# Kernel optimization log

Measured on AMD Instinct MI355X. Metric: run time of the kernel, lower is better.

Reference implementation:

```python
import jax, jax.numpy as jnp
import numpy as np

S, B, D = 2048, 2, 1024
H = 16
DH = D // H
FF = 4096
EPS = 1e-5


def _layernorm(x, g, b):
    mu = jnp.mean(x, axis=-1, keepdims=True)
    var = jnp.var(x, axis=-1, keepdims=True)
    return (x - mu) * jax.lax.rsqrt(var + EPS) * g + b


def setup_inputs() -> dict:
    key = jax.random.key(0)
    ks = jax.random.split(key, 8)
    scale = 1.0 / np.sqrt(D)
    return {
        "x": jax.random.normal(ks[0], (S, B, D), dtype=jnp.float32),
        "wq": jax.random.normal(ks[1], (D, D), dtype=jnp.float32) * scale,
        "wk": jax.random.normal(ks[2], (D, D), dtype=jnp.float32) * scale,
        "wv": jax.random.normal(ks[3], (D, D), dtype=jnp.float32) * scale,
        "wo": jax.random.normal(ks[4], (D, D), dtype=jnp.float32) * scale,
        "ln1_g": jnp.ones((D,), jnp.float32),
        "ln1_b": jnp.zeros((D,), jnp.float32),
        "ln2_g": jnp.ones((D,), jnp.float32),
        "ln2_b": jnp.zeros((D,), jnp.float32),
        "w1": jax.random.normal(ks[5], (D, FF), dtype=jnp.float32) * scale,
        "b1": jnp.zeros((FF,), jnp.float32),
        "w2": jax.random.normal(ks[6], (FF, D), dtype=jnp.float32) * (1.0 / np.sqrt(FF)),
        "b2": jnp.zeros((D,), jnp.float32),
    }


def reference(x, wq, wk, wv, wo, ln1_g, ln1_b, ln2_g, ln2_b, w1, b1, w2, b2):
    # --- sublayer 0: pre-LN multi-head self-attention with residual ---
    # original loops per timestep with mask=False, i.e. full (non-causal)
    # attention over the whole sequence; vectorized here.
    y = _layernorm(x, ln1_g, ln1_b)                      # [S,B,D]
    q = (y @ wq).reshape(S, B, H, DH)
    k = (y @ wk).reshape(S, B, H, DH)
    v = (y @ wv).reshape(S, B, H, DH)
    scores = jnp.einsum("sbhd,tbhd->bhst", q, k) / np.sqrt(DH)  # [B,H,S,S]
    attn = jax.nn.softmax(scores, axis=-1)
    ctx = jnp.einsum("bhst,tbhd->sbhd", attn, v).reshape(S, B, D)
    x = x + ctx @ wo

    # --- sublayer 1: pre-LN position-wise FFN with residual ---
    z = _layernorm(x, ln2_g, ln2_b)
    h = jax.nn.relu(z @ w1 + b1)
    return x + h @ w2 + b2
```

## Files before the change

### kernel.cpp

```cpp
#include <hip/hip_runtime.h>
#include <hip/hip_bf16.h>
#include <stdint.h>


#define S_LEN 2048
#define BATCH 2
#define DMODEL 1024
#define NHEAD 16
#define DHEAD 64
#define FFDIM 4096
#define MROWS (S_LEN * BATCH)

typedef unsigned short u16;
typedef __attribute__((ext_vector_type(8))) __bf16 bf16x8;
typedef __attribute__((ext_vector_type(4))) float f32x4;
typedef __attribute__((ext_vector_type(4))) u16 u16x4;

__device__ inline u16 f2bf(float f) {
  union { float f; unsigned u; } v; v.f = f;
  unsigned r = v.u + 0x7fffu + ((v.u >> 16) & 1u);
  return (u16)(r >> 16);
}

__device__ inline f32x4 mfma16(bf16x8 a, bf16x8 b, f32x4 c) {
  return __builtin_amdgcn_mfma_f32_16x16x32_bf16(a, b, c, 0, 0, 0);
}

__device__ inline void gload_lds16(const u16* g, u16* l) {
  __builtin_amdgcn_global_load_lds(
      (const __attribute__((address_space(1))) unsigned int*)g,
      (__attribute__((address_space(3))) unsigned int*)l, 16, 0, 0);
}

__device__ inline uint32_t cvt_pk_bf16(float lo, float hi) {
  uint32_t r;
  asm("v_cvt_pk_bf16_f32 %0, %1, %2" : "=v"(r) : "v"(lo), "v"(hi));
  return r;
}

__global__ __launch_bounds__(256) void ln_kernel(const float* __restrict__ x,
                                                 const float* __restrict__ gam,
                                                 const float* __restrict__ bet,
                                                 u16* __restrict__ out) {
  int row = blockIdx.x;
  int tid = threadIdx.x;
  const float4* xr = (const float4*)(x + (size_t)row * DMODEL);
  float4 v = xr[tid];
  float s = v.x + v.y + v.z + v.w;
  float ss = v.x * v.x + v.y * v.y + v.z * v.z + v.w * v.w;
#pragma unroll
  for (int m = 1; m < 64; m <<= 1) {
    s += __shfl_xor(s, m);
    ss += __shfl_xor(ss, m);
  }
  __shared__ float red[8];
  int w = tid >> 6, lane = tid & 63;
  if (lane == 0) { red[w] = s; red[4 + w] = ss; }
  __syncthreads();
  s = red[0] + red[1] + red[2] + red[3];
  ss = red[4] + red[5] + red[6] + red[7];
  float mu = s * (1.f / DMODEL);
  float var = ss * (1.f / DMODEL) - mu * mu;
  float rstd = rsqrtf(var + 1e-5f);
  float4 gv = ((const float4*)gam)[tid];
  float4 bv = ((const float4*)bet)[tid];
  u16x4 o;
  o.x = f2bf((v.x - mu) * rstd * gv.x + bv.x);
  o.y = f2bf((v.y - mu) * rstd * gv.y + bv.y);
  o.z = f2bf((v.z - mu) * rstd * gv.z + bv.z);
  o.w = f2bf((v.w - mu) * rstd * gv.w + bv.w);
  *(u16x4*)(out + (size_t)row * DMODEL + tid * 4) = o;
}

__global__ __launch_bounds__(256) void transpose_all(const float* __restrict__ wq,
                                                     const float* __restrict__ wk,
                                                     const float* __restrict__ wv,
                                                     const float* __restrict__ wo,
                                                     const float* __restrict__ w1,
                                                     const float* __restrict__ w2,
                                                     u16* __restrict__ wqkvt, u16* __restrict__ wot,
                                                     u16* __restrict__ w1t, u16* __restrict__ w2t) {
  int idx = blockIdx.x;
  const float* in;
  u16* out;
  int R, C;
  if (idx < 3072) {
    int which = idx >> 10;
    in = (which == 0) ? wq : (which == 1) ? wk : wv;
    out = wqkvt + (size_t)which * 1024 * 1024;
    R = 1024; C = 1024;
    idx &= 1023;
  } else if (idx < 4096) {
    in = wo; out = wot; R = 1024; C = 1024; idx -= 3072;
  } else if (idx < 8192) {
    in = w1; out = w1t; R = 1024; C = 4096; idx -= 4096;
  } else {
    in = w2; out = w2t; R = 4096; C = 1024; idx -= 8192;
  }
  int ntx = C >> 5;
  int tc = idx % ntx, tr = idx / ntx;
  int c0 = tc * 32, r0 = tr * 32;
  __shared__ u16 tile[32][33];
  int tx = threadIdx.x & 31, grp = threadIdx.x >> 5;
#pragma unroll
  for (int i = 0; i < 4; i++) {
    int r = grp * 4 + i;
    tile[r][tx] = f2bf(in[(size_t)(r0 + r) * C + c0 + tx]);
  }
  __syncthreads();
#pragma unroll
  for (int i = 0; i < 4; i++) {
    int rr = grp * 4 + i;
    out[(size_t)(c0 + rr) * R + r0 + tx] = tile[tx][rr];
  }
}

__global__ __launch_bounds__(256) void transpose_v(const u16* __restrict__ qkv,
                                                   u16* __restrict__ vt) {
  __shared__ u16 tile[32][33];
  int bh = blockIdx.z;
  int b = bh >> 4;
  int s0 = blockIdx.x * 32, d0 = blockIdx.y * 32;
  int h = bh & 15;
  int tx = threadIdx.x & 31, grp = threadIdx.x >> 5;
#pragma unroll
  for (int i = 0; i < 4; i++) {
    int sl = grp * 4 + i;
    tile[sl][tx] = qkv[(size_t)((s0 + sl) * BATCH + b) * 3072 + 2048 + h * DHEAD + d0 + tx];
  }
  __syncthreads();
#pragma unroll
  for (int i = 0; i < 4; i++) {
    int dl = grp * 4 + i;
    vt[((size_t)bh * DHEAD + d0 + dl) * S_LEN + s0 + tx] = tile[tx][dl];
  }
}

template <int MODE, int BN>
__global__ __launch_bounds__(256) void gemm_bt(const u16* __restrict__ A,
                                               const u16* __restrict__ Bt, void* __restrict__ Cout,
                                               const float* __restrict__ bias,
                                               const float* __restrict__ res, int M, int N, int K) {
  __shared__ __align__(16) u16 As[2][128 * 64];
  __shared__ __align__(16) u16 Bs[2][BN * 64];
  constexpr int NLOADS = 4 + BN / 32;

  int nwg = gridDim.x * gridDim.y;
  int f = blockIdx.y * gridDim.x + blockIdx.x;
  int nf = ((nwg & 7) == 0) ? ((f & 7) * (nwg >> 3) + (f >> 3)) : f;
  int bx = nf % gridDim.x, by = nf / gridDim.x;

  int bm0 = by * 128, bn0 = bx * BN;
  int tid = threadIdx.x, w = tid >> 6, lane = tid & 63;
  int g = lane >> 4, l15 = lane & 15;
  int lr = lane >> 3, ch = lane & 7;
  int srcch = (ch ^ lr) * 8;
  int wm = (w >> 1) * 64, wn = (w & 1) * (BN / 2);
  const int NJ = BN / 32;

  f32x4 acc[4][NJ];
#pragma unroll
  for (int i = 0; i < 4; i++)
#pragma unroll
    for (int j = 0; j < NJ; j++) {
      f32x4 z = {0.f, 0.f, 0.f, 0.f};
      acc[i][j] = z;
    }

  auto stage = [&](int k0, int buf) {
#pragma unroll
    for (int rd = 0; rd < 4; rd++) {
      int rb = (rd * 4 + w) * 8;
      gload_lds16(A + (size_t)(bm0 + rb + lr) * K + k0 + srcch, &As[buf][rb * 64]);
    }
#pragma unroll
    for (int rd = 0; rd < BN / 32; rd++) {
      int rb = (rd * 4 + w) * 8;
      gload_lds16(Bt + (size_t)(bn0 + rb + lr) * K + k0 + srcch, &Bs[buf][rb * 64]);
    }
  };

  int nkt = K >> 6;
  stage(0, 0);
  asm volatile("s_waitcnt vmcnt(0)" ::: "memory");
  __builtin_amdgcn_s_barrier();

  for (int kt = 0; kt < nkt; ++kt) {
    int cur = kt & 1;
    if (kt + 1 < nkt) {
      stage((kt + 1) << 6, cur ^ 1);
      asm volatile("s_waitcnt vmcnt(%0)" ::"n"(NLOADS) : "memory");
    } else {
      asm volatile("s_waitcnt vmcnt(0)" ::: "memory");
    }
    __builtin_amdgcn_s_barrier();
#pragma unroll
    for (int kk = 0; kk < 2; kk++) {
      bf16x8 af[4], bfr[NJ];
#pragma unroll
      for (int i = 0; i < 4; i++) {
        int row = wm + i * 16 + l15;
        af[i] = *(const bf16x8*)&As[cur][row * 64 + (((kk * 4 + g) ^ (row & 7)) * 8)];
      }
#pragma unroll
      for (int j = 0; j < NJ; j++) {
        int row = wn + j * 16 + l15;
        bfr[j] = *(const bf16x8*)&Bs[cur][row * 64 + (((kk * 4 + g) ^ (row & 7)) * 8)];
      }
#pragma unroll
      for (int i = 0; i < 4; i++)
#pragma unroll
        for (int j = 0; j < NJ; j++) acc[i][j] = mfma16(af[i], bfr[j], acc[i][j]);
    }
    __builtin_amdgcn_s_barrier();
  }

#pragma unroll
  for (int i = 0; i < 4; i++)
#pragma unroll
    for (int j = 0; j < NJ; j++) {
      int col = bn0 + wn + j * 16 + l15;
      float bval = (MODE == 2 || MODE == 3) ? bias[col] : 0.f;
#pragma unroll
      for (int r = 0; r < 4; r++) {
        int row = bm0 + wm + i * 16 + g * 4 + r;
        size_t idx = (size_t)row * N + col;
        float vacc = acc[i][j][r] + bval;
        if (MODE == 0)
          ((u16*)Cout)[idx] = f2bf(vacc);
        else if (MODE == 1)
          ((float*)Cout)[idx] = vacc + res[idx];
        else if (MODE == 2)
          ((u16*)Cout)[idx] = f2bf(fmaxf(vacc, 0.f));
        else
          ((float*)Cout)[idx] = vacc + res[idx];
      }
    }
}

__global__ __launch_bounds__(256) void attn_kernel(const u16* __restrict__ qkv,
                                                   const u16* __restrict__ vt,
                                                   u16* __restrict__ ctx) {
  int nwg = gridDim.x * gridDim.y;
  int f = blockIdx.y * gridDim.x + blockIdx.x;
  int nf = (f & 7) * (nwg >> 3) + (f >> 3);
  int qblk = nf % gridDim.x, bh = nf / gridDim.x;
  int b = bh >> 4, h = bh & 15;
  int tid = threadIdx.x, w = tid >> 6, lane = tid & 63;
  int g = lane >> 4, l15 = lane & 15;
  int lr = lane >> 3, ch = lane & 7;
  int q0 = qblk * 64 + w * 16;
  const float SCALE = 0.125f * 1.44269504f;

  __shared__ __align__(16) u16 ks[2][64 * 64];
  __shared__ __align__(16) u16 vs[2][64 * 64];

  bf16x8 qf0, qf1;
  {
    const u16* qp = qkv + ((size_t)(q0 + l15) * BATCH + b) * 3072 + h * DHEAD;
    qf0 = *(const bf16x8*)(qp + g * 8);
    qf1 = *(const bf16x8*)(qp + 32 + g * 8);
  }
  bf16x8 onef;
  {
    union { u16 u[8]; bf16x8 v; } ou;
#pragma unroll
    for (int i = 0; i < 8; i++) ou.u[i] = 0x3F80;
    onef = ou.v;
  }

  f32x4 accT[4];
#pragma unroll
  for (int n = 0; n < 4; n++) {
    f32x4 z = {0.f, 0.f, 0.f, 0.f};
    accT[n] = z;
  }
  f32x4 lacc = {0.f, 0.f, 0.f, 0.f};
  float negms = 0.f;

  auto stage = [&](int t0, int buf) {
#pragma unroll
    for (int rd = 0; rd < 2; rd++) {
      int rb = w * 16 + rd * 8;
      int row = rb + lr;
      const u16* ksrc =
          qkv + ((size_t)(t0 + row) * BATCH + b) * 3072 + 1024 + h * DHEAD + (ch ^ lr) * 8;
      gload_lds16(ksrc, &ks[buf][rb * 64]);
      const u16* vsrc = vt + ((size_t)bh * DHEAD + row) * S_LEN + t0 + (ch ^ lr) * 8;
      gload_lds16(vsrc, &vs[buf][rb * 64]);
    }
  };

  stage(0, 0);
  asm volatile("s_waitcnt vmcnt(0)" ::: "memory");
  __builtin_amdgcn_s_barrier();

  for (int it = 0; it < S_LEN / 64; ++it) {
    int cur = it & 1;
    if (it + 1 < S_LEN / 64) {
      stage((it + 1) * 64, cur ^ 1);
      asm volatile("s_waitcnt vmcnt(4)" ::: "memory");
    } else {
      asm volatile("s_waitcnt vmcnt(0)" ::: "memory");
    }
    __builtin_amdgcn_s_barrier();

    f32x4 scT[4];
#pragma unroll
    for (int tt = 0; tt < 4; tt++) {
      int row = tt * 16 + l15;
      bf16x8 kf0 = *(const bf16x8*)&ks[cur][row * 64 + ((g ^ (row & 7)) * 8)];
      bf16x8 kf1 = *(const bf16x8*)&ks[cur][row * 64 + (((4 + g) ^ (row & 7)) * 8)];
      f32x4 z = {0.f, 0.f, 0.f, 0.f};
      __builtin_amdgcn_s_setprio(1);
      z = mfma16(kf0, qf0, z);
      z = mfma16(kf1, qf1, z);
      __builtin_amdgcn_s_setprio(0);
      scT[tt] = z;
    }

    if (it == 0) {
      float pm = fmaxf(fmaxf(scT[0][0], scT[0][1]), fmaxf(scT[0][2], scT[0][3]));
#pragma unroll
      for (int tt = 1; tt < 4; tt++)
        pm = fmaxf(pm, fmaxf(fmaxf(scT[tt][0], scT[tt][1]), fmaxf(scT[tt][2], scT[tt][3])));
      pm = fmaxf(pm, __shfl_xor(pm, 16));
      pm = fmaxf(pm, __shfl_xor(pm, 32));
      negms = -pm * SCALE;
    }

    float p[4][4];
#pragma unroll
    for (int tt = 0; tt < 4; tt++)
#pragma unroll
      for (int r = 0; r < 4; r++) p[tt][r] = __builtin_amdgcn_exp2f(fmaf(scT[tt][r], SCALE, negms));

    uint32_t P32[4][2];
#pragma unroll
    for (int tt = 0; tt < 4; tt++)
#pragma unroll
      for (int m = 0; m < 2; m++) P32[tt][m] = cvt_pk_bf16(p[tt][2 * m], p[tt][2 * m + 1]);
#pragma unroll
    for (int t5 = 0; t5 < 2; t5++)
#pragma unroll
      for (int m = 0; m < 2; m++) {
        asm("v_permlane32_swap_b32 %0, %1" : "+v"(P32[2 * t5][m]), "+v"(P32[2 * t5 + 1][m]));
        asm("v_permlane16_swap_b32 %0, %1" : "+v"(P32[2 * t5][m]), "+v"(P32[2 * t5 + 1][m]));
      }
    bf16x8 pb[2];
#pragma unroll
    for (int s2 = 0; s2 < 2; s2++) {
      union { uint32_t u[4]; bf16x8 v; } uu;
      uu.u[0] = P32[2 * s2][0];
      uu.u[1] = P32[2 * s2][1];
      uu.u[2] = P32[2 * s2 + 1][0];
      uu.u[3] = P32[2 * s2 + 1][1];
      pb[s2] = uu.v;
    }

    __builtin_amdgcn_s_setprio(1);
    lacc = mfma16(onef, pb[0], lacc);
    lacc = mfma16(onef, pb[1], lacc);
    __builtin_amdgcn_s_setprio(0);
#pragma unroll
    for (int n = 0; n < 4; n++) {
      int vrow = n * 16 + l15;
      bf16x8 vf0 = *(const bf16x8*)&vs[cur][vrow * 64 + ((g ^ (vrow & 7)) * 8)];
      bf16x8 vf1 = *(const bf16x8*)&vs[cur][vrow * 64 + (((4 + g) ^ (vrow & 7)) * 8)];
      __builtin_amdgcn_s_setprio(1);
      accT[n] = mfma16(vf0, pb[0], accT[n]);
      accT[n] = mfma16(vf1, pb[1], accT[n]);
      __builtin_amdgcn_s_setprio(0);
    }
    __builtin_amdgcn_s_barrier();
  }

  float inv = 1.f / lacc[0];
  int srow = q0 + l15;
#pragma unroll
  for (int n = 0; n < 4; n++) {
    u16x4 o;
    o.x = f2bf(accT[n][0] * inv);
    o.y = f2bf(accT[n][1] * inv);
    o.z = f2bf(accT[n][2] * inv);
    o.w = f2bf(accT[n][3] * inv);
    *(u16x4*)(ctx + ((size_t)srow * BATCH + b) * DMODEL + h * DHEAD + n * 16 + 4 * g) = o;
  }
}

extern "C" void kernel_launch(void* const* d_in, const int* in_sizes, int n_in, void* d_out,
                              int out_size, void* d_ws, size_t ws_size, hipStream_t stream) {
  (void)in_sizes; (void)n_in; (void)out_size; (void)ws_size;
  const float* x    = (const float*)d_in[0];
  const float* wq   = (const float*)d_in[1];
  const float* wk   = (const float*)d_in[2];
  const float* wv   = (const float*)d_in[3];
  const float* wo   = (const float*)d_in[4];
  const float* ln1g = (const float*)d_in[5];
  const float* ln1b = (const float*)d_in[6];
  const float* ln2g = (const float*)d_in[7];
  const float* ln2b = (const float*)d_in[8];
  const float* w1   = (const float*)d_in[9];
  const float* b1   = (const float*)d_in[10];
  const float* w2   = (const float*)d_in[11];
  const float* b2   = (const float*)d_in[12];

  char* ws = (char*)d_ws;
  size_t off = 0;
  auto alloc = [&](size_t bytes) {
    void* p = ws + off;
    off += (bytes + 255) & ~(size_t)255;
    return p;
  };
  u16* yb    = (u16*)alloc((size_t)MROWS * DMODEL * 2);
  u16* wqkvt = (u16*)alloc((size_t)3072 * 1024 * 2);
  u16* wot   = (u16*)alloc((size_t)1024 * 1024 * 2);
  u16* w1t   = (u16*)alloc((size_t)4096 * 1024 * 2);
  u16* w2t   = (u16*)alloc((size_t)1024 * 4096 * 2);
  u16* qkvb  = (u16*)alloc((size_t)MROWS * 3072 * 2);
  u16* vtb   = (u16*)alloc((size_t)BATCH * NHEAD * DHEAD * S_LEN * 2);
  u16* ctxb  = (u16*)alloc((size_t)MROWS * DMODEL * 2);
  float* x1  = (float*)alloc((size_t)MROWS * DMODEL * 4);
  u16* zb    = (u16*)alloc((size_t)MROWS * DMODEL * 2);
  u16* hb    = (u16*)alloc((size_t)MROWS * FFDIM * 2);

  ln_kernel<<<MROWS, 256, 0, stream>>>(x, ln1g, ln1b, yb);
  transpose_all<<<12288, 256, 0, stream>>>(wq, wk, wv, wo, w1, w2, wqkvt, wot, w1t, w2t);

  gemm_bt<0, 128><<<dim3(3072 / 128, 4096 / 128), 256, 0, stream>>>(yb, wqkvt, qkvb, nullptr,
                                                                    nullptr, 4096, 3072, 1024);
  transpose_v<<<dim3(64, 2, 32), 256, 0, stream>>>(qkvb, vtb);
  attn_kernel<<<dim3(32, 32), 256, 0, stream>>>(qkvb, vtb, ctxb);
  gemm_bt<1, 64><<<dim3(16, 32), 256, 0, stream>>>(ctxb, wot, x1, nullptr, x, 4096, 1024, 1024);

  ln_kernel<<<MROWS, 256, 0, stream>>>(x1, ln2g, ln2b, zb);
  gemm_bt<2, 128><<<dim3(32, 32), 256, 0, stream>>>(zb, w1t, hb, b1, nullptr, 4096, 4096, 1024);
  gemm_bt<3, 64><<<dim3(16, 32), 256, 0, stream>>>(hb, w2t, d_out, b2, x1, 4096, 1024, 4096);
}
```

Baseline: 245.4 us.

## Add 256x256-tile 8-wave GEMM for QKV and FFN1 projections

Adds a new GEMM kernel with 256x256 output tiles, 512 threads (8 waves) and double-buffered LDS. It interleaves prefetch of the next K-tile in quarters with MFMA compute, using setprio and barriers. The QKV and FFN-up projections now use this kernel, so each tile reuses more data and fewer global/LDS loads are needed per FLOP. The trade-offs are higher register pressure (32 accumulators per wave), about 128KB of LDS per block and fewer workgroups (192 and 256), which may underfill the CUs. The old gemm_bt epilogue is reduced to its residual-add modes.

```diff
diff --git a/kernel.cpp b/kernel.cpp
--- a/kernel.cpp
+++ b/kernel.cpp
@@ -136,6 +136,115 @@
   }
 }
 
+template <int MODE>
+__global__ __launch_bounds__(512, 2) void gemm8(const u16* __restrict__ A,
+                                                const u16* __restrict__ Bt,
+                                                void* __restrict__ Cout,
+                                                const float* __restrict__ bias, int M, int N,
+                                                int K) {
+  __shared__ __align__(16) u16 As[2][256 * 64];
+  __shared__ __align__(16) u16 Bs[2][256 * 64];
+
+  int nwgx = gridDim.x;
+  int nwg = nwgx * gridDim.y;
+  int f = blockIdx.y * nwgx + blockIdx.x;
+  int nf = (f & 7) * (nwg >> 3) + (f >> 3);
+  int bx = nf % nwgx, by = nf / nwgx;
+  int bm0 = by * 256, bn0 = bx * 256;
+  int tid = threadIdx.x, w = tid >> 6, lane = tid & 63;
+  int g = lane >> 4, l15 = lane & 15;
+  int lr = lane >> 3, ch = lane & 7;
+  int srcch = (ch ^ lr) * 8;
+  int wm = (w >> 2) * 128, wn = (w & 3) * 64;
+
+  f32x4 acc[8][4];
+#pragma unroll
+  for (int i = 0; i < 8; i++)
+#pragma unroll
+    for (int j = 0; j < 4; j++) {
+      f32x4 z = {0.f, 0.f, 0.f, 0.f};
+      acc[i][j] = z;
+    }
+
+  auto stageHalf = [&](int t, int hh) {
+    int k0 = t << 6;
+    int buf = t & 1;
+    const u16* src = (hh < 2) ? A : Bt;
+    u16* dstbase = (hh < 2) ? As[buf] : Bs[buf];
+    int base0 = (hh < 2) ? bm0 : bn0;
+    int h = hh & 1;
+#pragma unroll
+    for (int rd = 0; rd < 2; rd++) {
+      int rb = h * 128 + w * 16 + rd * 8;
+      gload_lds16(src + (size_t)(base0 + rb + lr) * K + k0 + srcch, &dstbase[rb * 64]);
+    }
+  };
+
+  int nkt = K >> 6;
+#pragma unroll
+  for (int hh = 0; hh < 4; hh++) stageHalf(0, hh);
+  asm volatile("s_waitcnt vmcnt(0)" ::: "memory");
+  __builtin_amdgcn_s_barrier();
+
+  for (int t = 0; t < nkt; ++t) {
+    int cur = t & 1;
+    bool pf = (t + 1 < nkt);
+#pragma unroll
+    for (int q = 0; q < 4; q++) {
+      if (pf) stageHalf(t + 1, q);
+      if (q == 0) {
+        if (pf)
+          asm volatile("s_waitcnt vmcnt(2)" ::: "memory");
+        else
+          asm volatile("s_waitcnt vmcnt(0)" ::: "memory");
+        __builtin_amdgcn_s_barrier();
+      }
+      bf16x8 af[4][2], bfr[2][2];
+#pragma unroll
+      for (int i = 0; i < 4; i++) {
+        int row = wm + (q & 1) * 64 + i * 16 + l15;
+#pragma unroll
+        for (int ks = 0; ks < 2; ks++)
+          af[i][ks] = *(const bf16x8*)&As[cur][row * 64 + (((ks * 4 + g) ^ (row & 7)) * 8)];
+      }
+#pragma unroll
+      for (int j = 0; j < 2; j++) {
+        int row = wn + (q >> 1) * 32 + j * 16 + l15;
+#pragma unroll
+        for (int ks = 0; ks < 2; ks++)
+          bfr[j][ks] = *(const bf16x8*)&Bs[cur][row * 64 + (((ks * 4 + g) ^ (row & 7)) * 8)];
+      }
+      __builtin_amdgcn_s_barrier();
+      __builtin_amdgcn_s_setprio(1);
+#pragma unroll
+      for (int ks = 0; ks < 2; ks++)
+#pragma unroll
+        for (int i = 0; i < 4; i++)
+#pragma unroll
+          for (int j = 0; j < 2; j++)
+            acc[(q & 1) * 4 + i][(q >> 1) * 2 + j] =
+                mfma16(af[i][ks], bfr[j][ks], acc[(q & 1) * 4 + i][(q >> 1) * 2 + j]);
+      __builtin_amdgcn_s_setprio(0);
+      __builtin_amdgcn_s_barrier();
+    }
+  }
+
+#pragma unroll
+  for (int n2 = 0; n2 < 4; n2++) {
+    int col = bn0 + wn + n2 * 16 + l15;
+    float bval = (MODE == 2) ? bias[col] : 0.f;
+#pragma unroll
+    for (int m2 = 0; m2 < 8; m2++)
+#pragma unroll
+      for (int r = 0; r < 4; r++) {
+        int row = bm0 + wm + m2 * 16 + g * 4 + r;
+        float v = acc[m2][n2][r] + bval;
+        if (MODE == 2) v = fmaxf(v, 0.f);
+        ((u16*)Cout)[(size_t)row * N + col] = f2bf(v);
+      }
+  }
+}
+
 template <int MODE, int BN>
 __global__ __launch_bounds__(256) void gemm_bt(const u16* __restrict__ A,
                                                const u16* __restrict__ Bt, void* __restrict__ Cout,
@@ -220,20 +329,12 @@
 #pragma unroll
     for (int j = 0; j < NJ; j++) {
       int col = bn0 + wn + j * 16 + l15;
-      float bval = (MODE == 2 || MODE == 3) ? bias[col] : 0.f;
+      float bval = (MODE == 3) ? bias[col] : 0.f;
 #pragma unroll
       for (int r = 0; r < 4; r++) {
         int row = bm0 + wm + i * 16 + g * 4 + r;
         size_t idx = (size_t)row * N + col;
-        float vacc = acc[i][j][r] + bval;
-        if (MODE == 0)
-          ((u16*)Cout)[idx] = f2bf(vacc);
-        else if (MODE == 1)
-          ((float*)Cout)[idx] = vacc + res[idx];
-        else if (MODE == 2)
-          ((u16*)Cout)[idx] = f2bf(fmaxf(vacc, 0.f));
-        else
-          ((float*)Cout)[idx] = vacc + res[idx];
+        ((float*)Cout)[idx] = acc[i][j][r] + bval + res[idx];
       }
     }
 }
@@ -427,13 +528,13 @@
   ln_kernel<<<MROWS, 256, 0, stream>>>(x, ln1g, ln1b, yb);
   transpose_all<<<12288, 256, 0, stream>>>(wq, wk, wv, wo, w1, w2, wqkvt, wot, w1t, w2t);
 
-  gemm_bt<0, 128><<<dim3(3072 / 128, 4096 / 128), 256, 0, stream>>>(yb, wqkvt, qkvb, nullptr,
-                                                                    nullptr, 4096, 3072, 1024);
+  gemm8<0><<<dim3(3072 / 256, 4096 / 256), 512, 0, stream>>>(yb, wqkvt, qkvb, nullptr, 4096, 3072,
+                                                             1024);
   transpose_v<<<dim3(64, 2, 32), 256, 0, stream>>>(qkvb, vtb);
   attn_kernel<<<dim3(32, 32), 256, 0, stream>>>(qkvb, vtb, ctxb);
   gemm_bt<1, 64><<<dim3(16, 32), 256, 0, stream>>>(ctxb, wot, x1, nullptr, x, 4096, 1024, 1024);
 
   ln_kernel<<<MROWS, 256, 0, stream>>>(x1, ln2g, ln2b, zb);
-  gemm_bt<2, 128><<<dim3(32, 32), 256, 0, stream>>>(zb, w1t, hb, b1, nullptr, 4096, 4096, 1024);
+  gemm8<2><<<dim3(4096 / 256, 4096 / 256), 512, 0, stream>>>(zb, w1t, hb, b1, 4096, 4096, 1024);
   gemm_bt<3, 64><<<dim3(16, 32), 256, 0, stream>>>(hb, w2t, d_out, b2, x1, 4096, 1024, 4096);
 }
```

Measured after the change: 281.3 us. +14.6%, slower.

## Software-pipeline PV MFMAs one iteration behind QK in attention loop

Applied to the files above, without the earlier changes.

The attention inner loop now defers the P·V and row-sum MFMAs by one iteration. The current tile's V fragments and bf16 P values are held in registers and consumed after the next tile's QK^T MFMAs, with a drain step after the loop. The aim is to overlap the exp/pack/permlane work with matrix-core work and hide LDS read latency. In exchange it raises register pressure (V fragments plus P carried across iterations) and adds an explicit lgkmcnt wait before the barrier.

```diff
diff --git a/kernel.cpp b/kernel.cpp
--- a/kernel.cpp
+++ b/kernel.cpp
@@ -277,6 +277,8 @@
   }
   f32x4 lacc = {0.f, 0.f, 0.f, 0.f};
   float negms = 0.f;
+  bf16x8 pbp[2];
+  bf16x8 vfp[4][2];
 
   auto stage = [&](int t0, int buf) {
 #pragma unroll
@@ -319,6 +321,25 @@
       scT[tt] = z;
     }
 
+    if (it > 0) {
+      __builtin_amdgcn_s_setprio(1);
+      lacc = mfma16(onef, pbp[0], lacc);
+      lacc = mfma16(onef, pbp[1], lacc);
+#pragma unroll
+      for (int n = 0; n < 4; n++) {
+        accT[n] = mfma16(vfp[n][0], pbp[0], accT[n]);
+        accT[n] = mfma16(vfp[n][1], pbp[1], accT[n]);
+      }
+      __builtin_amdgcn_s_setprio(0);
+    }
+
+#pragma unroll
+    for (int n = 0; n < 4; n++) {
+      int vrow = n * 16 + l15;
+      vfp[n][0] = *(const bf16x8*)&vs[cur][vrow * 64 + ((g ^ (vrow & 7)) * 8)];
+      vfp[n][1] = *(const bf16x8*)&vs[cur][vrow * 64 + (((4 + g) ^ (vrow & 7)) * 8)];
+    }
+
     if (it == 0) {
       float pm = fmaxf(fmaxf(scT[0][0], scT[0][1]), fmaxf(scT[0][2], scT[0][3]));
 #pragma unroll
@@ -328,13 +349,11 @@
       pm = fmaxf(pm, __shfl_xor(pm, 32));
       negms = -pm * SCALE;
     }
-
     float p[4][4];
 #pragma unroll
     for (int tt = 0; tt < 4; tt++)
 #pragma unroll
       for (int r = 0; r < 4; r++) p[tt][r] = __builtin_amdgcn_exp2f(fmaf(scT[tt][r], SCALE, negms));
-
     uint32_t P32[4][2];
 #pragma unroll
     for (int tt = 0; tt < 4; tt++)
@@ -347,7 +366,6 @@
         asm("v_permlane32_swap_b32 %0, %1" : "+v"(P32[2 * t5][m]), "+v"(P32[2 * t5 + 1][m]));
         asm("v_permlane16_swap_b32 %0, %1" : "+v"(P32[2 * t5][m]), "+v"(P32[2 * t5 + 1][m]));
       }
-    bf16x8 pb[2];
 #pragma unroll
     for (int s2 = 0; s2 < 2; s2++) {
       union { uint32_t u[4]; bf16x8 v; } uu;
@@ -355,24 +373,19 @@
       uu.u[1] = P32[2 * s2][1];
       uu.u[2] = P32[2 * s2 + 1][0];
       uu.u[3] = P32[2 * s2 + 1][1];
-      pb[s2] = uu.v;
-    }
-
-    __builtin_amdgcn_s_setprio(1);
-    lacc = mfma16(onef, pb[0], lacc);
-    lacc = mfma16(onef, pb[1], lacc);
-    __builtin_amdgcn_s_setprio(0);
-#pragma unroll
-    for (int n = 0; n < 4; n++) {
-      int vrow = n * 16 + l15;
-      bf16x8 vf0 = *(const bf16x8*)&vs[cur][vrow * 64 + ((g ^ (vrow & 7)) * 8)];
-      bf16x8 vf1 = *(const bf16x8*)&vs[cur][vrow * 64 + (((4 + g) ^ (vrow & 7)) * 8)];
-      __builtin_amdgcn_s_setprio(1);
-      accT[n] = mfma16(vf0, pb[0], accT[n]);
-      accT[n] = mfma16(vf1, pb[1], accT[n]);
-      __builtin_amdgcn_s_setprio(0);
-    }
+      pbp[s2] = uu.v;
+    }
+
+    asm volatile("s_waitcnt lgkmcnt(0)" ::: "memory");
     __builtin_amdgcn_s_barrier();
+  }
+
+  lacc = mfma16(onef, pbp[0], lacc);
+  lacc = mfma16(onef, pbp[1], lacc);
+#pragma unroll
+  for (int n = 0; n < 4; n++) {
+    accT[n] = mfma16(vfp[n][0], pbp[0], accT[n]);
+    accT[n] = mfma16(vfp[n][1], pbp[1], accT[n]);
   }
 
   float inv = 1.f / lacc[0];
```

New measurement: 243.6 us. Within noise of the previous version (-0.7%).
